# Performance work log

Hardware: AMD Instinct MI355X
Metric: run time of the kernel (lower is better)

The kernel has to match this reference:

```python
import jax, jax.numpy as jnp
import numpy as np

N_OBJ, N_EVT, N_EDGE, N_MAIN = 50000, 100000, 500000, 25000
OBJ_DIM, EVT_DIM = 256, 256


def setup_inputs() -> dict:
    key = jax.random.key(0)
    ks = jax.random.split(key, 12)
    s = 1.0 / np.sqrt(OBJ_DIM)
    return {
        "object_X": jax.random.normal(ks[0], (N_OBJ, OBJ_DIM), jnp.float32),
        "event_X": jax.random.normal(ks[1], (N_EVT, EVT_DIM), jnp.float32),
        "lc_obj_idx": jax.random.randint(ks[2], (N_EDGE,), 0, N_OBJ),
        "lc_evt_idx": jax.random.randint(ks[3], (N_EDGE,), 0, N_EVT),
        "main_idx": jax.random.randint(ks[4], (N_MAIN,), 0, N_OBJ),
        # lifecycle_proj: Linear(event_dim, obj_dim)
        "W_proj": jax.random.uniform(ks[5], (OBJ_DIM, EVT_DIM), jnp.float32, -s, s),
        "b_proj": jax.random.uniform(ks[6], (OBJ_DIM,), jnp.float32, -s, s),
        # GRUCell(obj_dim, obj_dim): weight_ih/hh are [3*H, H]
        "W_ih": jax.random.uniform(ks[7], (3 * OBJ_DIM, OBJ_DIM), jnp.float32, -s, s),
        "b_ih": jax.random.uniform(ks[8], (3 * OBJ_DIM,), jnp.float32, -s, s),
        "W_hh": jax.random.uniform(ks[9], (3 * OBJ_DIM, OBJ_DIM), jnp.float32, -s, s),
        "b_hh": jax.random.uniform(ks[10], (3 * OBJ_DIM,), jnp.float32, -s, s),
    }


def reference(object_X, event_X, lc_obj_idx, lc_evt_idx, main_idx,
              W_proj, b_proj, W_ih, b_ih, W_hh, b_hh):
    n_obj = object_X.shape[0]
    # gather event feats, linear + ReLU  -> [E, obj_dim]
    proj = jax.nn.relu(event_X[lc_evt_idx] @ W_proj.T + b_proj)
    # scatter_mean over target objects (empty slots -> 0, like torch_scatter)
    sums = jax.ops.segment_sum(proj, lc_obj_idx, num_segments=n_obj)
    cnt = jax.ops.segment_sum(jnp.ones((lc_obj_idx.shape[0],), proj.dtype),
                              lc_obj_idx, num_segments=n_obj)
    profile = sums / jnp.maximum(cnt, 1.0)[:, None]  # [N_obj, obj_dim]
    # GRUCell(profile, object_X)
    gi = profile @ W_ih.T + b_ih   # [N_obj, 3H]
    gh = object_X @ W_hh.T + b_hh  # [N_obj, 3H]
    i_r, i_z, i_n = jnp.split(gi, 3, axis=-1)
    h_r, h_z, h_n = jnp.split(gh, 3, axis=-1)
    r = jax.nn.sigmoid(i_r + h_r)
    z = jax.nn.sigmoid(i_z + h_z)
    n = jnp.tanh(i_n + r * h_n)
    updated = (1.0 - z) * n + z * object_X
    # masked blend: only main objects take updated values
    mask = jnp.zeros((n_obj, 1), object_X.dtype).at[main_idx].set(1.0)
    return mask * updated + (1.0 - mask) * object_X
```

## Files before the change

### kernel.cpp

```cpp
#include <hip/hip_runtime.h>

typedef unsigned short u16;
typedef __attribute__((ext_vector_type(8))) short bf16x8;
typedef __attribute__((ext_vector_type(4))) float f32x4;

struct __align__(8) u16x4_t { u16 x, y, z, w; };

__device__ __forceinline__ float b2f(u16 b) {
  union { unsigned u; float f; } v; v.u = ((unsigned)b) << 16; return v.f;
}
__device__ __forceinline__ u16 f2b(float f) {
  union { float f; unsigned u; } v; v.f = f;
  unsigned r = v.u + 0x7fffu + ((v.u >> 16) & 1u);
  return (u16)(r >> 16);
}
__device__ __forceinline__ unsigned pk2(float x, float y) {
  union { float f; unsigned u; } a, b; a.f = x; b.f = y;
  return __builtin_amdgcn_perm(b.u + 0x8000u, a.u + 0x8000u, 0x07060302u);
}
__device__ __forceinline__ bf16x8 pack8(float4 lo, float4 hi) {
  union { bf16x8 v; unsigned u[4]; } t;
  t.u[0] = pk2(lo.x, lo.y); t.u[1] = pk2(lo.z, lo.w);
  t.u[2] = pk2(hi.x, hi.y); t.u[3] = pk2(hi.z, hi.w);
  return t.v;
}

__global__ void init_misc(const float* __restrict__ Wp, const float* __restrict__ Wi,
                          const float* __restrict__ Wh, u16* __restrict__ wb,
                          const int* __restrict__ main_idx, int* __restrict__ mask,
                          int* __restrict__ mlist, int* __restrict__ cpos,
                          int* __restrict__ mcount, int nMain) {
  int b = blockIdx.x;
  if (b < 448) {
    int t = b * 256 + threadIdx.x;
    const float* src; int o;
    if (t < 16384)      { src = Wp; o = t; }
    else if (t < 65536) { src = Wi; o = t - 16384; }
    else                { src = Wh; o = t - 65536; }
    float4 v = ((const float4*)src)[o];
    u16x4_t q;
    q.x = f2b(v.x); q.y = f2b(v.y); q.z = f2b(v.z); q.w = f2b(v.w);
    ((u16x4_t*)wb)[t] = q;
  } else {
    int t = (b - 448) * 256 + threadIdx.x;
    if (t < nMain) {
      int o = main_idx[t];
      if (atomicCAS(&mask[o], 0, 1) == 0) {
        int i = atomicAdd(mcount, 1);
        mlist[i] = o;
        cpos[o] = i;
      }
    }
  }
}

__global__ void count_edges(const int* __restrict__ obj_idx, const int* __restrict__ mask,
                            int* __restrict__ deg, int n) {
  int e = blockIdx.x * 256 + threadIdx.x;
  if (e >= n) return;
  int o = obj_idx[e];
  if (mask[o]) atomicAdd(&deg[o], 1);
}

__global__ __launch_bounds__(256)
void alloc_offs(const int* __restrict__ mlist, const int* __restrict__ mcount,
                const int* __restrict__ deg, int* __restrict__ offs,
                int* __restrict__ tcur, int* __restrict__ rrows, int Mpad) {
  int i = blockIdx.x * 256 + threadIdx.x;
  int lane = threadIdx.x & 63;
  int mc = *mcount;
  if (i < Mpad) rrows[i] = (i < mc) ? mlist[i] : 0;
  int o = (i < mc) ? mlist[i] : 0;
  int d = (i < mc) ? deg[o] : 0;
  int x = d;
#pragma unroll
  for (int s = 1; s < 64; s <<= 1) {
    int y = __shfl_up(x, s, 64);
    if (lane >= s) x += y;
  }
  int wt = __shfl(x, 63, 64);
  int base = 0;
  if (lane == 63 && wt > 0) base = atomicAdd(tcur, wt);
  base = __shfl(base, 63, 64);
  if (i < mc) offs[o] = base + (x - d);
}

__global__ void fill_edges(const int* __restrict__ obj_idx, const int* __restrict__ evt_idx,
                           const int* __restrict__ mask, const int* __restrict__ offs,
                           int* __restrict__ cursor, int* __restrict__ elist, int n) {
  int e = blockIdx.x * 256 + threadIdx.x;
  if (e >= n) return;
  int o = obj_idx[e];
  if (!mask[o]) return;
  int pos = atomicAdd(&cursor[o], 1);
  elist[offs[o] + pos] = evt_idx[e];
}

__global__ __launch_bounds__(256)
void accum_prof(const u16* __restrict__ P, const int* __restrict__ elist,
                const int* __restrict__ offs, const int* __restrict__ deg,
                const int* __restrict__ mlist, const int* __restrict__ mcount,
                u16* __restrict__ prof, int Mpad) {
  const int wave = threadIdx.x >> 6;
  const int lane = threadIdx.x & 63;
  const int i = blockIdx.x * 4 + wave;
  if (i >= Mpad) return;
  const int mc = *mcount;
  float a0 = 0.f, a1 = 0.f, a2 = 0.f, a3 = 0.f;
  int d = 0;
  if (i < mc) {
    const int o = mlist[i];
    const int off = offs[o];
    d = deg[o];
    int j = 0;
    for (; j + 1 < d; j += 2) {
      int e0 = elist[off + j], e1 = elist[off + j + 1];
      u16x4_t p0 = *(const u16x4_t*)(P + (size_t)e0 * 256 + lane * 4);
      u16x4_t p1 = *(const u16x4_t*)(P + (size_t)e1 * 256 + lane * 4);
      a0 += b2f(p0.x) + b2f(p1.x);
      a1 += b2f(p0.y) + b2f(p1.y);
      a2 += b2f(p0.z) + b2f(p1.z);
      a3 += b2f(p0.w) + b2f(p1.w);
    }
    if (j < d) {
      int e0 = elist[off + j];
      u16x4_t p0 = *(const u16x4_t*)(P + (size_t)e0 * 256 + lane * 4);
      a0 += b2f(p0.x); a1 += b2f(p0.y); a2 += b2f(p0.z); a3 += b2f(p0.w);
    }
  }
  float s = 1.f / fmaxf((float)d, 1.f);
  u16x4_t ov;
  ov.x = f2b(a0 * s); ov.y = f2b(a1 * s); ov.z = f2b(a2 * s); ov.w = f2b(a3 * s);
  *(u16x4_t*)(prof + (size_t)i * 256 + lane * 4) = ov;
}

template<int RELU, int GATHER, int AF32>
__global__ __launch_bounds__(256, 2)
void gemm_rs(const u16* __restrict__ Ab, const float* __restrict__ Af,
             const u16* __restrict__ B, const float* __restrict__ bias,
             u16* __restrict__ C, const int* __restrict__ ridx, int M, int N) {
  __shared__ u16 lB[128 * 256];
  const int tid  = threadIdx.x;
  const int lane = tid & 63;
  const int wave = tid >> 6;
  const int m0 = blockIdx.x * 128;
  const int n0 = blockIdx.y * 128;
  const int mR = (wave & 1) * 64;
  const int nC = (wave >> 1) * 64;
  const int la15 = lane & 15;
  const int kof  = (lane >> 4) * 8;

  int arow[4];
#pragma unroll
  for (int i = 0; i < 4; ++i) {
    int r = m0 + mR + i * 16 + la15;
    if (GATHER) arow[i] = ridx[r];
    else        arow[i] = (r < M) ? r : (M - 1);
  }

#pragma unroll
  for (int s = 0; s < 16; ++s) {
    int seg = s * 256 + tid;
    int row = seg >> 5;
    int cp  = seg & 31;
    int c   = (cp & 24) | ((cp ^ row) & 7);
    const u16* gB = B + (size_t)(n0 + row) * 256 + c * 8;
    __builtin_amdgcn_global_load_lds(
        (const __attribute__((address_space(1))) void*)gB,
        (__attribute__((address_space(3))) void*)(lB + s * 2048 + wave * 512),
        16, 0, 0);
  }
  __syncthreads();

  f32x4 acc[4][4] = {};

  const float* ap[4];
  const u16*   abp[4];
  float4 c0[4], c1[4];
  if (AF32) {
#pragma unroll
    for (int i = 0; i < 4; ++i) {
      ap[i] = Af + (size_t)arow[i] * 256 + kof;
      c0[i] = *(const float4*)(ap[i]);
      c1[i] = *(const float4*)(ap[i] + 4);
    }
  } else {
#pragma unroll
    for (int i = 0; i < 4; ++i) abp[i] = Ab + (size_t)arow[i] * 256 + kof;
  }

#pragma unroll
  for (int ks = 0; ks < 8; ++ks) {
    bf16x8 af[4], bfr[4];
    if (AF32) {
      float4 n0v[4], n1v[4];
      if (ks < 7) {
#pragma unroll
        for (int i = 0; i < 4; ++i) {
          n0v[i] = *(const float4*)(ap[i] + (ks + 1) * 32);
          n1v[i] = *(const float4*)(ap[i] + (ks + 1) * 32 + 4);
        }
      }
#pragma unroll
      for (int i = 0; i < 4; ++i) af[i] = pack8(c0[i], c1[i]);
      if (ks < 7) {
#pragma unroll
        for (int i = 0; i < 4; ++i) { c0[i] = n0v[i]; c1[i] = n1v[i]; }
      }
    } else {
#pragma unroll
      for (int i = 0; i < 4; ++i)
        af[i] = *(const bf16x8*)(abp[i] + ks * 32);
    }
#pragma unroll
    for (int j = 0; j < 4; ++j) {
      int rj = nC + j * 16 + la15;
      int c  = ks * 4 + (lane >> 4);
      int cp = (c & 24) | ((c ^ rj) & 7);
      bfr[j] = *(const bf16x8*)(lB + rj * 256 + cp * 8);
    }
#pragma unroll
    for (int i = 0; i < 4; ++i)
#pragma unroll
      for (int j = 0; j < 4; ++j)
        acc[i][j] = __builtin_amdgcn_mfma_f32_16x16x32_bf16(af[i], bfr[j], acc[i][j], 0, 0, 0);
  }

  const int crow = (lane >> 4) * 4;
#pragma unroll
  for (int i = 0; i < 4; ++i) {
#pragma unroll
    for (int j = 0; j < 4; ++j) {
      int col = n0 + nC + j * 16 + la15;
      float bv = bias[col];
#pragma unroll
      for (int q = 0; q < 4; ++q) {
        int row = m0 + mR + i * 16 + crow + q;
        if (row < M) {
          float v = acc[i][j][q] + bv;
          if (RELU) v = fmaxf(v, 0.f);
          C[(size_t)row * N + col] = f2b(v);
        }
      }
    }
  }
}

__global__ __launch_bounds__(256)
void gate_out(const u16* __restrict__ gi, const u16* __restrict__ gh,
              const float* __restrict__ objX, const int* __restrict__ mask,
              const int* __restrict__ cpos, float* __restrict__ out, int nObj) {
  const int wave = threadIdx.x >> 6;
  const int lane = threadIdx.x & 63;
  const int row = blockIdx.x * 4 + wave;
  if (row >= nObj) return;
  float4 x4 = *(const float4*)(objX + (size_t)row * 256 + lane * 4);
  float4 r4 = x4;
  if (mask[row]) {
    size_t b = (size_t)cpos[row] * 768 + lane * 4;
    u16x4_t ir = *(const u16x4_t*)(gi + b);
    u16x4_t iz = *(const u16x4_t*)(gi + b + 256);
    u16x4_t in_ = *(const u16x4_t*)(gi + b + 512);
    u16x4_t hr = *(const u16x4_t*)(gh + b);
    u16x4_t hz = *(const u16x4_t*)(gh + b + 256);
    u16x4_t hn = *(const u16x4_t*)(gh + b + 512);
    float xs[4] = {x4.x, x4.y, x4.z, x4.w};
    u16 irs[4] = {ir.x, ir.y, ir.z, ir.w};
    u16 izs[4] = {iz.x, iz.y, iz.z, iz.w};
    u16 ins[4] = {in_.x, in_.y, in_.z, in_.w};
    u16 hrs[4] = {hr.x, hr.y, hr.z, hr.w};
    u16 hzs[4] = {hz.x, hz.y, hz.z, hz.w};
    u16 hns[4] = {hn.x, hn.y, hn.z, hn.w};
    float rs[4];
#pragma unroll
    for (int q = 0; q < 4; ++q) {
      float r = 1.f / (1.f + __expf(-(b2f(irs[q]) + b2f(hrs[q]))));
      float z = 1.f / (1.f + __expf(-(b2f(izs[q]) + b2f(hzs[q]))));
      float a = b2f(ins[q]) + r * b2f(hns[q]);
      float n = 1.f - 2.f / (__expf(2.f * a) + 1.f);
      rs[q] = (1.f - z) * n + z * xs[q];
    }
    r4.x = rs[0]; r4.y = rs[1]; r4.z = rs[2]; r4.w = rs[3];
  }
  *(float4*)(out + (size_t)row * 256 + lane * 4) = r4;
}


extern "C" void kernel_launch(void* const* d_in, const int* in_sizes, int n_in,
                              void* d_out, int out_size, void* d_ws, size_t ws_size,
                              hipStream_t stream) {
  const float* objX   = (const float*)d_in[0];
  const float* evtX   = (const float*)d_in[1];
  const int* obj_idx  = (const int*)d_in[2];
  const int* evt_idx  = (const int*)d_in[3];
  const int* main_idx = (const int*)d_in[4];
  const float* Wp = (const float*)d_in[5];
  const float* bp = (const float*)d_in[6];
  const float* Wi = (const float*)d_in[7];
  const float* bi = (const float*)d_in[8];
  const float* Wh = (const float*)d_in[9];
  const float* bh = (const float*)d_in[10];

  const int nObj  = in_sizes[0] / 256;
  const int nEvt  = in_sizes[1] / 256;
  const int nEdge = in_sizes[2];
  const int nMain = in_sizes[4];
  const int Mpad  = ((nMain + 127) / 128) * 128;

  char* ws = (char*)d_ws;
  u16*   P     = (u16*)(ws + 0);
  u16*   gi    = (u16*)(ws + 0);
  u16*   gh    = (u16*)(ws + 51200000);
  u16*   prof  = (u16*)(ws + 89735168);
  u16*   wb    = (u16*)(ws + 102580224);
  u16*   wpb   = wb;
  u16*   wib   = wb + 65536;
  u16*   whb   = wb + 262144;
  int*   deg   = (int*)(ws + 103497728);
  int*   cursor= (int*)(ws + 103697728);
  int*   mask  = (int*)(ws + 103897728);
  int*   mcount= (int*)(ws + 104097728);
  int*   tcur  = (int*)(ws + 104097792);
  int*   cpos  = (int*)(ws + 104097856);
  int*   offs  = (int*)(ws + 104297856);
  int*   mlist = (int*)(ws + 104497856);
  int*   rrows = (int*)(ws + 104598208);
  int*   elist = (int*)(ws + 104698560);
  float* out   = (float*)d_out;

  hipMemsetAsync(ws + 103497728, 0, 600128, stream);

  init_misc<<<546, 256, 0, stream>>>(Wp, Wi, Wh, wb, main_idx, mask, mlist, cpos, mcount, nMain);

  gemm_rs<1, 0, 1><<<dim3((nEvt + 127) / 128, 2), 256, 0, stream>>>(
      nullptr, evtX, wpb, bp, P, nullptr, nEvt, 256);

  count_edges<<<(nEdge + 255) / 256, 256, 0, stream>>>(obj_idx, mask, deg, nEdge);
  alloc_offs<<<Mpad / 256, 256, 0, stream>>>(mlist, mcount, deg, offs, tcur, rrows, Mpad);
  fill_edges<<<(nEdge + 255) / 256, 256, 0, stream>>>(obj_idx, evt_idx, mask, offs, cursor, elist, nEdge);

  accum_prof<<<(Mpad + 3) / 4, 256, 0, stream>>>(P, elist, offs, deg, mlist, mcount, prof, Mpad);

  gemm_rs<0, 0, 0><<<dim3(Mpad / 128, 6), 256, 0, stream>>>(
      prof, nullptr, wib, bi, gi, nullptr, Mpad, 768);
  gemm_rs<0, 1, 1><<<dim3(Mpad / 128, 6), 256, 0, stream>>>(
      nullptr, objX, whb, bh, gh, rrows, Mpad, 768);

  gate_out<<<(nObj + 3) / 4, 256, 0, stream>>>(gi, gh, objX, mask, cpos, out, nObj);
}
```

Baseline: 440.7 us.

## Make GEMMs persistent with resident B tile and stream A rows

The GEMM kernel becomes persistent. Each block loads its 128-column B tile into LDS once, then loops over row chunks of 64 with a fixed grid (256 or 85 blocks in x), and each wave covers 16 rows by all 128 columns. The next chunk's A rows are prefetched into registers. The aim is to spread the B-tile load across many row tiles and reduce launch and tail overhead. A separate gather_cvt kernel now pre-gathers the main objects' rows of object_X and converts them to bf16, so the gh GEMM reads contiguous bf16 instead of gathered fp32. Each wave's tile is smaller, which lowers per-wave data reuse, and gather_cvt adds an extra kernel launch and buffer.

```diff
diff --git a/kernel.cpp b/kernel.cpp
--- a/kernel.cpp
+++ b/kernel.cpp
@@ -94,6 +94,19 @@
   if (!mask[o]) return;
   int pos = atomicAdd(&cursor[o], 1);
   elist[offs[o] + pos] = evt_idx[e];
+}
+
+__global__ __launch_bounds__(256)
+void gather_cvt(const float* __restrict__ objX, const int* __restrict__ rrows,
+                u16* __restrict__ objc, int Mpad) {
+  int row = blockIdx.x * 4 + (threadIdx.x >> 6);
+  int lane = threadIdx.x & 63;
+  if (row >= Mpad) return;
+  int src = rrows[row];
+  float4 v = *(const float4*)(objX + (size_t)src * 256 + lane * 4);
+  u16x4_t o;
+  o.x = f2b(v.x); o.y = f2b(v.y); o.z = f2b(v.z); o.w = f2b(v.w);
+  *(u16x4_t*)(objc + (size_t)row * 256 + lane * 4) = o;
 }
 
 __global__ __launch_bounds__(256)
@@ -134,29 +147,18 @@
   *(u16x4_t*)(prof + (size_t)i * 256 + lane * 4) = ov;
 }
 
-template<int RELU, int GATHER, int AF32>
+template<int RELU, int AF32>
 __global__ __launch_bounds__(256, 2)
-void gemm_rs(const u16* __restrict__ Ab, const float* __restrict__ Af,
-             const u16* __restrict__ B, const float* __restrict__ bias,
-             u16* __restrict__ C, const int* __restrict__ ridx, int M, int N) {
+void gemm_stream(const u16* __restrict__ Ab, const float* __restrict__ Af,
+                 const u16* __restrict__ B, const float* __restrict__ bias,
+                 u16* __restrict__ C, int M, int N, int nIter, int rowStride) {
   __shared__ u16 lB[128 * 256];
   const int tid  = threadIdx.x;
   const int lane = tid & 63;
   const int wave = tid >> 6;
-  const int m0 = blockIdx.x * 128;
-  const int n0 = blockIdx.y * 128;
-  const int mR = (wave & 1) * 64;
-  const int nC = (wave >> 1) * 64;
+  const int n0   = blockIdx.y * 128;
   const int la15 = lane & 15;
-  const int kof  = (lane >> 4) * 8;
-
-  int arow[4];
-#pragma unroll
-  for (int i = 0; i < 4; ++i) {
-    int r = m0 + mR + i * 16 + la15;
-    if (GATHER) arow[i] = ridx[r];
-    else        arow[i] = (r < M) ? r : (M - 1);
-  }
+  const int kof8 = (lane >> 4) * 8;
 
 #pragma unroll
   for (int s = 0; s < 16; ++s) {
@@ -172,72 +174,79 @@
   }
   __syncthreads();
 
-  f32x4 acc[4][4] = {};
-
-  const float* ap[4];
-  const u16*   abp[4];
-  float4 c0[4], c1[4];
-  if (AF32) {
-#pragma unroll
-    for (int i = 0; i < 4; ++i) {
-      ap[i] = Af + (size_t)arow[i] * 256 + kof;
-      c0[i] = *(const float4*)(ap[i]);
-      c1[i] = *(const float4*)(ap[i] + 4);
-    }
-  } else {
-#pragma unroll
-    for (int i = 0; i < 4; ++i) abp[i] = Ab + (size_t)arow[i] * 256 + kof;
-  }
-
-#pragma unroll
-  for (int ks = 0; ks < 8; ++ks) {
-    bf16x8 af[4], bfr[4];
+  float4 va[8][2];
+  bf16x8 vb[8];
+
+  {
+    int rb = blockIdx.x * 64 + wave * 16;
+    int ar = rb + la15; ar = (ar < M) ? ar : (M - 1);
     if (AF32) {
-      float4 n0v[4], n1v[4];
-      if (ks < 7) {
-#pragma unroll
-        for (int i = 0; i < 4; ++i) {
-          n0v[i] = *(const float4*)(ap[i] + (ks + 1) * 32);
-          n1v[i] = *(const float4*)(ap[i] + (ks + 1) * 32 + 4);
+      const float* ap = Af + (size_t)ar * 256 + kof8;
+#pragma unroll
+      for (int ks = 0; ks < 8; ++ks) {
+        va[ks][0] = *(const float4*)(ap + ks * 32);
+        va[ks][1] = *(const float4*)(ap + ks * 32 + 4);
+      }
+    } else {
+      const u16* ap = Ab + (size_t)ar * 256 + kof8;
+#pragma unroll
+      for (int ks = 0; ks < 8; ++ks) vb[ks] = *(const bf16x8*)(ap + ks * 32);
+    }
+  }
+
+  const int crow = (lane >> 4) * 4;
+
+  for (int t = 0; t < nIter; ++t) {
+    const int rb = t * rowStride + blockIdx.x * 64 + wave * 16;
+
+    bf16x8 cur[8];
+    if (AF32) {
+#pragma unroll
+      for (int ks = 0; ks < 8; ++ks) cur[ks] = pack8(va[ks][0], va[ks][1]);
+    } else {
+#pragma unroll
+      for (int ks = 0; ks < 8; ++ks) cur[ks] = vb[ks];
+    }
+
+    if (t + 1 < nIter) {
+      int rb2 = (t + 1) * rowStride + blockIdx.x * 64 + wave * 16;
+      int ar = rb2 + la15; ar = (ar < M) ? ar : (M - 1);
+      if (AF32) {
+        const float* ap = Af + (size_t)ar * 256 + kof8;
+#pragma unroll
+        for (int ks = 0; ks < 8; ++ks) {
+          va[ks][0] = *(const float4*)(ap + ks * 32);
+          va[ks][1] = *(const float4*)(ap + ks * 32 + 4);
         }
-      }
-#pragma unroll
-      for (int i = 0; i < 4; ++i) af[i] = pack8(c0[i], c1[i]);
-      if (ks < 7) {
-#pragma unroll
-        for (int i = 0; i < 4; ++i) { c0[i] = n0v[i]; c1[i] = n1v[i]; }
-      }
-    } else {
-#pragma unroll
-      for (int i = 0; i < 4; ++i)
-        af[i] = *(const bf16x8*)(abp[i] + ks * 32);
-    }
-#pragma unroll
-    for (int j = 0; j < 4; ++j) {
-      int rj = nC + j * 16 + la15;
-      int c  = ks * 4 + (lane >> 4);
-      int cp = (c & 24) | ((c ^ rj) & 7);
-      bfr[j] = *(const bf16x8*)(lB + rj * 256 + cp * 8);
-    }
-#pragma unroll
-    for (int i = 0; i < 4; ++i)
-#pragma unroll
-      for (int j = 0; j < 4; ++j)
-        acc[i][j] = __builtin_amdgcn_mfma_f32_16x16x32_bf16(af[i], bfr[j], acc[i][j], 0, 0, 0);
-  }
-
-  const int crow = (lane >> 4) * 4;
-#pragma unroll
-  for (int i = 0; i < 4; ++i) {
-#pragma unroll
-    for (int j = 0; j < 4; ++j) {
-      int col = n0 + nC + j * 16 + la15;
+      } else {
+        const u16* ap = Ab + (size_t)ar * 256 + kof8;
+#pragma unroll
+        for (int ks = 0; ks < 8; ++ks) vb[ks] = *(const bf16x8*)(ap + ks * 32);
+      }
+    }
+
+    f32x4 acc[8] = {};
+#pragma unroll
+    for (int ks = 0; ks < 8; ++ks) {
+#pragma unroll
+      for (int j = 0; j < 8; ++j) {
+        int rj = j * 16 + la15;
+        int c  = ks * 4 + (lane >> 4);
+        int cp = (c & 24) | ((c ^ rj) & 7);
+        bf16x8 bfr = *(const bf16x8*)(lB + rj * 256 + cp * 8);
+        acc[j] = __builtin_amdgcn_mfma_f32_16x16x32_bf16(cur[ks], bfr, acc[j], 0, 0, 0);
+      }
+    }
+
+#pragma unroll
+    for (int j = 0; j < 8; ++j) {
+      int col = n0 + j * 16 + la15;
       float bv = bias[col];
 #pragma unroll
       for (int q = 0; q < 4; ++q) {
-        int row = m0 + mR + i * 16 + crow + q;
+        int row = rb + crow + q;
         if (row < M) {
-          float v = acc[i][j][q] + bv;
+          float v = acc[j][q] + bv;
           if (RELU) v = fmaxf(v, 0.f);
           C[(size_t)row * N + col] = f2b(v);
         }
@@ -312,39 +321,50 @@
   u16*   gi    = (u16*)(ws + 0);
   u16*   gh    = (u16*)(ws + 51200000);
   u16*   prof  = (u16*)(ws + 89735168);
-  u16*   wb    = (u16*)(ws + 102580224);
+  u16*   objc  = (u16*)(ws + 102580224);
+  u16*   wb    = (u16*)(ws + 115425280);
   u16*   wpb   = wb;
   u16*   wib   = wb + 65536;
   u16*   whb   = wb + 262144;
-  int*   deg   = (int*)(ws + 103497728);
-  int*   cursor= (int*)(ws + 103697728);
-  int*   mask  = (int*)(ws + 103897728);
-  int*   mcount= (int*)(ws + 104097728);
-  int*   tcur  = (int*)(ws + 104097792);
-  int*   cpos  = (int*)(ws + 104097856);
-  int*   offs  = (int*)(ws + 104297856);
-  int*   mlist = (int*)(ws + 104497856);
-  int*   rrows = (int*)(ws + 104598208);
-  int*   elist = (int*)(ws + 104698560);
+  int*   deg   = (int*)(ws + 116342784);
+  int*   cursor= (int*)(ws + 116542784);
+  int*   mask  = (int*)(ws + 116742784);
+  int*   mcount= (int*)(ws + 116942784);
+  int*   tcur  = (int*)(ws + 116942848);
+  int*   cpos  = (int*)(ws + 116942912);
+  int*   offs  = (int*)(ws + 117142912);
+  int*   mlist = (int*)(ws + 117342912);
+  int*   rrows = (int*)(ws + 117443264);
+  int*   elist = (int*)(ws + 117543616);
   float* out   = (float*)d_out;
 
-  hipMemsetAsync(ws + 103497728, 0, 600128, stream);
+  hipMemsetAsync(ws + 116342784, 0, 600128, stream);
 
   init_misc<<<546, 256, 0, stream>>>(Wp, Wi, Wh, wb, main_idx, mask, mlist, cpos, mcount, nMain);
 
-  gemm_rs<1, 0, 1><<<dim3((nEvt + 127) / 128, 2), 256, 0, stream>>>(
-      nullptr, evtX, wpb, bp, P, nullptr, nEvt, 256);
+  {
+    const int gx = 256, rowStride = gx * 64;
+    const int nIter = (nEvt + rowStride - 1) / rowStride;
+    gemm_stream<1, 1><<<dim3(gx, 2), 256, 0, stream>>>(
+        nullptr, evtX, wpb, bp, P, nEvt, 256, nIter, rowStride);
+  }
 
   count_edges<<<(nEdge + 255) / 256, 256, 0, stream>>>(obj_idx, mask, deg, nEdge);
   alloc_offs<<<Mpad / 256, 256, 0, stream>>>(mlist, mcount, deg, offs, tcur, rrows, Mpad);
   fill_edges<<<(nEdge + 255) / 256, 256, 0, stream>>>(obj_idx, evt_idx, mask, offs, cursor, elist, nEdge);
 
+  gather_cvt<<<(Mpad + 3) / 4, 256, 0, stream>>>(objX, rrows, objc, Mpad);
+
   accum_prof<<<(Mpad + 3) / 4, 256, 0, stream>>>(P, elist, offs, deg, mlist, mcount, prof, Mpad);
 
-  gemm_rs<0, 0, 0><<<dim3(Mpad / 128, 6), 256, 0, stream>>>(
-      prof, nullptr, wib, bi, gi, nullptr, Mpad, 768);
-  gemm_rs<0, 1, 1><<<dim3(Mpad / 128, 6), 256, 0, stream>>>(
-      nullptr, objX, whb, bh, gh, rrows, Mpad, 768);
+  {
+    const int gx = 85, rowStride = gx * 64;
+    const int nIter = (Mpad + rowStride - 1) / rowStride;
+    gemm_stream<0, 0><<<dim3(gx, 6), 256, 0, stream>>>(
+        prof, nullptr, wib, bi, gi, Mpad, 768, nIter, rowStride);
+    gemm_stream<0, 0><<<dim3(gx, 6), 256, 0, stream>>>(
+        objc, nullptr, whb, bh, gh, Mpad, 768, nIter, rowStride);
+  }
 
   gate_out<<<(nObj + 3) / 4, 256, 0, stream>>>(gi, gh, objX, mask, cpos, out, nObj);
 }
```

New measurement: 559.7 us. +27.0%, slower.

## Pre-convert event features to bf16 and stage both GEMM operands through LDS

Applied to the files above, without the earlier changes.

A new prep kernel converts the whole event feature matrix to bf16 up front. The GEMMs are restructured to load both A and B tiles into LDS in 64-wide K chunks with global_load_lds, instead of holding all of B in LDS and reading A directly from global fp32 memory. The object-feature row gather and its bf16 conversion move into the profile accumulation kernel, and the two GRU GEMMs are merged into one launch. The cost is an extra full pass over the event matrix, a larger workspace, more synchronisation points per K-loop, and LDS reads with no swizzle, which may cause bank conflicts.

```diff
diff --git a/kernel.cpp b/kernel.cpp
--- a/kernel.cpp
+++ b/kernel.cpp
@@ -14,25 +14,23 @@
   unsigned r = v.u + 0x7fffu + ((v.u >> 16) & 1u);
   return (u16)(r >> 16);
 }
-__device__ __forceinline__ unsigned pk2(float x, float y) {
-  union { float f; unsigned u; } a, b; a.f = x; b.f = y;
-  return __builtin_amdgcn_perm(b.u + 0x8000u, a.u + 0x8000u, 0x07060302u);
-}
-__device__ __forceinline__ bf16x8 pack8(float4 lo, float4 hi) {
-  union { bf16x8 v; unsigned u[4]; } t;
-  t.u[0] = pk2(lo.x, lo.y); t.u[1] = pk2(lo.z, lo.w);
-  t.u[2] = pk2(hi.x, hi.y); t.u[3] = pk2(hi.z, hi.w);
-  return t.v;
-}
-
-__global__ void init_misc(const float* __restrict__ Wp, const float* __restrict__ Wi,
-                          const float* __restrict__ Wh, u16* __restrict__ wb,
-                          const int* __restrict__ main_idx, int* __restrict__ mask,
-                          int* __restrict__ mlist, int* __restrict__ cpos,
-                          int* __restrict__ mcount, int nMain) {
+
+__global__ void prep(const float* __restrict__ evtX, u16* __restrict__ evtb, int nEvtF4,
+                     const float* __restrict__ Wp, const float* __restrict__ Wi,
+                     const float* __restrict__ Wh, u16* __restrict__ wb,
+                     const int* __restrict__ main_idx, int* __restrict__ mask,
+                     int* __restrict__ mlist, int* __restrict__ cpos,
+                     int* __restrict__ mcount, int nMain) {
+  const int cvtBlocks = nEvtF4 / 256;
   int b = blockIdx.x;
-  if (b < 448) {
+  if (b < cvtBlocks) {
     int t = b * 256 + threadIdx.x;
+    float4 v = ((const float4*)evtX)[t];
+    u16x4_t o;
+    o.x = f2b(v.x); o.y = f2b(v.y); o.z = f2b(v.z); o.w = f2b(v.w);
+    ((u16x4_t*)evtb)[t] = o;
+  } else if (b < cvtBlocks + 448) {
+    int t = (b - cvtBlocks) * 256 + threadIdx.x;
     const float* src; int o;
     if (t < 16384)      { src = Wp; o = t; }
     else if (t < 65536) { src = Wi; o = t - 16384; }
@@ -42,7 +40,7 @@
     q.x = f2b(v.x); q.y = f2b(v.y); q.z = f2b(v.z); q.w = f2b(v.w);
     ((u16x4_t*)wb)[t] = q;
   } else {
-    int t = (b - 448) * 256 + threadIdx.x;
+    int t = (b - cvtBlocks - 448) * 256 + threadIdx.x;
     if (t < nMain) {
       int o = main_idx[t];
       if (atomicCAS(&mask[o], 0, 1) == 0) {
@@ -97,14 +95,19 @@
 }
 
 __global__ __launch_bounds__(256)
-void accum_prof(const u16* __restrict__ P, const int* __restrict__ elist,
-                const int* __restrict__ offs, const int* __restrict__ deg,
-                const int* __restrict__ mlist, const int* __restrict__ mcount,
-                u16* __restrict__ prof, int Mpad) {
+void accum_gather(const u16* __restrict__ P, const int* __restrict__ elist,
+                  const int* __restrict__ offs, const int* __restrict__ deg,
+                  const int* __restrict__ mlist, const int* __restrict__ mcount,
+                  const float* __restrict__ objX, const int* __restrict__ rrows,
+                  u16* __restrict__ prof, u16* __restrict__ objc, int Mpad) {
   const int wave = threadIdx.x >> 6;
   const int lane = threadIdx.x & 63;
   const int i = blockIdx.x * 4 + wave;
   if (i >= Mpad) return;
+
+  int src = rrows[i];
+  float4 xv = *(const float4*)(objX + (size_t)src * 256 + lane * 4);
+
   const int mc = *mcount;
   float a0 = 0.f, a1 = 0.f, a2 = 0.f, a3 = 0.f;
   int d = 0;
@@ -129,109 +132,74 @@
     }
   }
   float s = 1.f / fmaxf((float)d, 1.f);
+  u16x4_t pv;
+  pv.x = f2b(a0 * s); pv.y = f2b(a1 * s); pv.z = f2b(a2 * s); pv.w = f2b(a3 * s);
+  *(u16x4_t*)(prof + (size_t)i * 256 + lane * 4) = pv;
+
   u16x4_t ov;
-  ov.x = f2b(a0 * s); ov.y = f2b(a1 * s); ov.z = f2b(a2 * s); ov.w = f2b(a3 * s);
-  *(u16x4_t*)(prof + (size_t)i * 256 + lane * 4) = ov;
-}
-
-template<int RELU, int GATHER, int AF32>
-__global__ __launch_bounds__(256, 2)
-void gemm_rs(const u16* __restrict__ Ab, const float* __restrict__ Af,
-             const u16* __restrict__ B, const float* __restrict__ bias,
-             u16* __restrict__ C, const int* __restrict__ ridx, int M, int N) {
-  __shared__ u16 lB[128 * 256];
+  ov.x = f2b(xv.x); ov.y = f2b(xv.y); ov.z = f2b(xv.z); ov.w = f2b(xv.w);
+  *(u16x4_t*)(objc + (size_t)i * 256 + lane * 4) = ov;
+}
+
+template<int RELU>
+__device__ __forceinline__
+void gemm_core(const u16* __restrict__ A, const u16* __restrict__ B,
+               const float* __restrict__ bias, u16* __restrict__ C,
+               int M, int N, int n0, u16* lA, u16* lB) {
   const int tid  = threadIdx.x;
   const int lane = tid & 63;
   const int wave = tid >> 6;
   const int m0 = blockIdx.x * 128;
-  const int n0 = blockIdx.y * 128;
   const int mR = (wave & 1) * 64;
   const int nC = (wave >> 1) * 64;
-  const int la15 = lane & 15;
-  const int kof  = (lane >> 4) * 8;
-
-  int arow[4];
+
+  f32x4 acc[4][4] = {};
+
+  for (int kt = 0; kt < 256; kt += 64) {
+    __syncthreads();
+#pragma unroll
+    for (int s = 0; s < 4; ++s) {
+      int slot = s * 256 + tid;
+      int row  = slot >> 3;
+      int kk   = (slot & 7) * 8;
+      int ar = m0 + row; ar = (ar < M) ? ar : (M - 1);
+      const u16* gA = A + (size_t)ar * 256 + (kt + kk);
+      __builtin_amdgcn_global_load_lds(
+          (const __attribute__((address_space(1))) void*)gA,
+          (__attribute__((address_space(3))) void*)(lA + s * 2048 + wave * 512),
+          16, 0, 0);
+      const u16* gB = B + (size_t)(n0 + row) * 256 + (kt + kk);
+      __builtin_amdgcn_global_load_lds(
+          (const __attribute__((address_space(1))) void*)gB,
+          (__attribute__((address_space(3))) void*)(lB + s * 2048 + wave * 512),
+          16, 0, 0);
+    }
+    __syncthreads();
+
+#pragma unroll
+    for (int ks = 0; ks < 2; ++ks) {
+      const int kb = ks * 32 + (lane >> 4) * 8;
+      bf16x8 af[4], bfr[4];
+#pragma unroll
+      for (int i = 0; i < 4; ++i) {
+        af[i]  = *(const bf16x8*)(lA + (mR + i * 16 + (lane & 15)) * 64 + kb);
+        bfr[i] = *(const bf16x8*)(lB + (nC + i * 16 + (lane & 15)) * 64 + kb);
+      }
+#pragma unroll
+      for (int i = 0; i < 4; ++i)
+#pragma unroll
+        for (int j = 0; j < 4; ++j)
+          acc[i][j] = __builtin_amdgcn_mfma_f32_16x16x32_bf16(af[i], bfr[j], acc[i][j], 0, 0, 0);
+    }
+  }
+
+  const int crow = (lane >> 4) * 4;
+  const int ccol = lane & 15;
 #pragma unroll
   for (int i = 0; i < 4; ++i) {
-    int r = m0 + mR + i * 16 + la15;
-    if (GATHER) arow[i] = ridx[r];
-    else        arow[i] = (r < M) ? r : (M - 1);
-  }
-
-#pragma unroll
-  for (int s = 0; s < 16; ++s) {
-    int seg = s * 256 + tid;
-    int row = seg >> 5;
-    int cp  = seg & 31;
-    int c   = (cp & 24) | ((cp ^ row) & 7);
-    const u16* gB = B + (size_t)(n0 + row) * 256 + c * 8;
-    __builtin_amdgcn_global_load_lds(
-        (const __attribute__((address_space(1))) void*)gB,
-        (__attribute__((address_space(3))) void*)(lB + s * 2048 + wave * 512),
-        16, 0, 0);
-  }
-  __syncthreads();
-
-  f32x4 acc[4][4] = {};
-
-  const float* ap[4];
-  const u16*   abp[4];
-  float4 c0[4], c1[4];
-  if (AF32) {
-#pragma unroll
-    for (int i = 0; i < 4; ++i) {
-      ap[i] = Af + (size_t)arow[i] * 256 + kof;
-      c0[i] = *(const float4*)(ap[i]);
-      c1[i] = *(const float4*)(ap[i] + 4);
-    }
-  } else {
-#pragma unroll
-    for (int i = 0; i < 4; ++i) abp[i] = Ab + (size_t)arow[i] * 256 + kof;
-  }
-
-#pragma unroll
-  for (int ks = 0; ks < 8; ++ks) {
-    bf16x8 af[4], bfr[4];
-    if (AF32) {
-      float4 n0v[4], n1v[4];
-      if (ks < 7) {
-#pragma unroll
-        for (int i = 0; i < 4; ++i) {
-          n0v[i] = *(const float4*)(ap[i] + (ks + 1) * 32);
-          n1v[i] = *(const float4*)(ap[i] + (ks + 1) * 32 + 4);
-        }
-      }
-#pragma unroll
-      for (int i = 0; i < 4; ++i) af[i] = pack8(c0[i], c1[i]);
-      if (ks < 7) {
-#pragma unroll
-        for (int i = 0; i < 4; ++i) { c0[i] = n0v[i]; c1[i] = n1v[i]; }
-      }
-    } else {
-#pragma unroll
-      for (int i = 0; i < 4; ++i)
-        af[i] = *(const bf16x8*)(abp[i] + ks * 32);
-    }
 #pragma unroll
     for (int j = 0; j < 4; ++j) {
-      int rj = nC + j * 16 + la15;
-      int c  = ks * 4 + (lane >> 4);
-      int cp = (c & 24) | ((c ^ rj) & 7);
-      bfr[j] = *(const bf16x8*)(lB + rj * 256 + cp * 8);
-    }
-#pragma unroll
-    for (int i = 0; i < 4; ++i)
-#pragma unroll
-      for (int j = 0; j < 4; ++j)
-        acc[i][j] = __builtin_amdgcn_mfma_f32_16x16x32_bf16(af[i], bfr[j], acc[i][j], 0, 0, 0);
-  }
-
-  const int crow = (lane >> 4) * 4;
-#pragma unroll
-  for (int i = 0; i < 4; ++i) {
-#pragma unroll
-    for (int j = 0; j < 4; ++j) {
-      int col = n0 + nC + j * 16 + la15;
+      int col = n0 + nC + j * 16 + ccol;
       float bv = bias[col];
 #pragma unroll
       for (int q = 0; q < 4; ++q) {
@@ -244,6 +212,26 @@
       }
     }
   }
+}
+
+__global__ __launch_bounds__(256, 2)
+void gemm_p(const u16* __restrict__ A, const u16* __restrict__ B,
+            const float* __restrict__ bias, u16* __restrict__ C, int M) {
+  __shared__ u16 lA[128 * 64];
+  __shared__ u16 lB[128 * 64];
+  gemm_core<1>(A, B, bias, C, M, 256, blockIdx.y * 128, lA, lB);
+}
+
+__global__ __launch_bounds__(256, 2)
+void gemm2_dual(const u16* __restrict__ prof, const u16* __restrict__ objc,
+                const u16* __restrict__ wib, const u16* __restrict__ whb,
+                const float* __restrict__ bi, const float* __restrict__ bh,
+                u16* __restrict__ gi, u16* __restrict__ gh, int Mpad) {
+  __shared__ u16 lA[128 * 64];
+  __shared__ u16 lB[128 * 64];
+  int y = blockIdx.y;
+  if (y < 6) gemm_core<0>(prof, wib, bi, gi, Mpad, 768, y * 128, lA, lB);
+  else       gemm_core<0>(objc, whb, bh, gh, Mpad, 768, (y - 6) * 128, lA, lB);
 }
 
 __global__ __launch_bounds__(256)
@@ -312,39 +300,41 @@
   u16*   gi    = (u16*)(ws + 0);
   u16*   gh    = (u16*)(ws + 51200000);
   u16*   prof  = (u16*)(ws + 89735168);
-  u16*   wb    = (u16*)(ws + 102580224);
+  u16*   objc  = (u16*)(ws + 102580224);
+  u16*   evtb  = (u16*)(ws + 115425280);
+  u16*   wb    = (u16*)(ws + 166625280);
   u16*   wpb   = wb;
   u16*   wib   = wb + 65536;
   u16*   whb   = wb + 262144;
-  int*   deg   = (int*)(ws + 103497728);
-  int*   cursor= (int*)(ws + 103697728);
-  int*   mask  = (int*)(ws + 103897728);
-  int*   mcount= (int*)(ws + 104097728);
-  int*   tcur  = (int*)(ws + 104097792);
-  int*   cpos  = (int*)(ws + 104097856);
-  int*   offs  = (int*)(ws + 104297856);
-  int*   mlist = (int*)(ws + 104497856);
-  int*   rrows = (int*)(ws + 104598208);
-  int*   elist = (int*)(ws + 104698560);
+  int*   deg   = (int*)(ws + 167542784);
+  int*   cursor= (int*)(ws + 167742784);
+  int*   mask  = (int*)(ws + 167942784);
+  int*   mcount= (int*)(ws + 168142784);
+  int*   tcur  = (int*)(ws + 168142848);
+  int*   cpos  = (int*)(ws + 168142912);
+  int*   offs  = (int*)(ws + 168342912);
+  int*   mlist = (int*)(ws + 168542912);
+  int*   rrows = (int*)(ws + 168643264);
+  int*   elist = (int*)(ws + 168743616);
   float* out   = (float*)d_out;
 
-  hipMemsetAsync(ws + 103497728, 0, 600128, stream);
-
-  init_misc<<<546, 256, 0, stream>>>(Wp, Wi, Wh, wb, main_idx, mask, mlist, cpos, mcount, nMain);
-
-  gemm_rs<1, 0, 1><<<dim3((nEvt + 127) / 128, 2), 256, 0, stream>>>(
-      nullptr, evtX, wpb, bp, P, nullptr, nEvt, 256);
+  hipMemsetAsync(ws + 167542784, 0, 600128, stream);
+
+  const int nEvtF4 = in_sizes[1] / 4;
+  const int prepGrid = nEvtF4 / 256 + 448 + (nMain + 255) / 256;
+  prep<<<prepGrid, 256, 0, stream>>>(evtX, evtb, nEvtF4, Wp, Wi, Wh, wb,
+                                     main_idx, mask, mlist, cpos, mcount, nMain);
+
+  gemm_p<<<dim3((nEvt + 127) / 128, 2), 256, 0, stream>>>(evtb, wpb, bp, P, nEvt);
 
   count_edges<<<(nEdge + 255) / 256, 256, 0, stream>>>(obj_idx, mask, deg, nEdge);
   alloc_offs<<<Mpad / 256, 256, 0, stream>>>(mlist, mcount, deg, offs, tcur, rrows, Mpad);
   fill_edges<<<(nEdge + 255) / 256, 256, 0, stream>>>(obj_idx, evt_idx, mask, offs, cursor, elist, nEdge);
 
-  accum_prof<<<(Mpad + 3) / 4, 256, 0, stream>>>(P, elist, offs, deg, mlist, mcount, prof, Mpad);
-
-  gemm_rs<0, 0, 0><<<dim3(Mpad / 128, 6), 256, 0, stream>>>(
-      prof, nullptr, wib, bi, gi, nullptr, Mpad, 768);
-  gemm_rs<0, 1, 1><<<dim3(Mpad / 128, 6), 256, 0, stream>>>(
-      nullptr, objX, whb, bh, gh, rrows, Mpad, 768);
+  accum_gather<<<(Mpad + 3) / 4, 256, 0, stream>>>(P, elist, offs, deg, mlist, mcount,
+                                                   objX, rrows, prof, objc, Mpad);
+
+  gemm2_dual<<<dim3(Mpad / 128, 12), 256, 0, stream>>>(prof, objc, wib, whb, bi, bh, gi, gh, Mpad);
 
   gate_out<<<(nObj + 3) / 4, 256, 0, stream>>>(gi, gh, objX, mask, cpos, out, nObj);
 }
```

Result: faster. 377.5 us (-14.4%).
